# Performance work log

Hardware: AMD Instinct MI355X
Metric: run time of the kernel (lower is better)

## Reference

```python
import jax, jax.numpy as jnp
import numpy as np
import math

N_NODES = 50000
N_EDGES = 800000
IN_CH = 128
HID_CH = 16   # per-head channels of conv1
OUT_CH = 1    # per-head channels of conv2 (forced so Linear(heads,100) type-checks)
HEADS = 8


def _seg_softmax(scores, seg, n):
    # softmax over edges grouped by target node (variable-size neighborhoods)
    m = jax.ops.segment_max(scores, seg, num_segments=n)
    e = jnp.exp(scores - m[seg])
    s = jax.ops.segment_sum(e, seg, num_segments=n)
    return e / (s[seg] + 1e-16)


def _transformer_conv(x, edge_index, Wq, bq, Wk, bk, Wv, bv, Ws, bs, heads, ch):
    # PyG TransformerConv, concat=True, root_weight=True, beta=False
    n = x.shape[0]
    src, dst = edge_index[0], edge_index[1]
    q = (x @ Wq + bq).reshape(n, heads, ch)
    k = (x @ Wk + bk).reshape(n, heads, ch)
    v = (x @ Wv + bv).reshape(n, heads, ch)
    qi = q[dst]              # [E, H, C] gather at target
    kj = k[src]              # [E, H, C] gather at source
    vj = v[src]              # [E, H, C]
    alpha = jnp.einsum('ehc,ehc->eh', qi, kj) / math.sqrt(ch)  # [E, H]
    alpha = _seg_softmax(alpha, dst, n)
    agg = jax.ops.segment_sum(vj * alpha[:, :, None], dst, num_segments=n)
    out = agg.reshape(n, heads * ch)
    return out + x @ Ws + bs   # skip connection lin_skip(x)


def setup_inputs() -> dict:
    key = jax.random.key(0)
    ks = jax.random.split(key, 16)
    s = 0.05
    d1 = HEADS * HID_CH  # 128
    d2 = HEADS * OUT_CH  # 8
    inp = {
        'x': jax.random.normal(ks[0], (N_NODES, IN_CH), dtype=jnp.float32),
        'edge_index': jax.random.randint(ks[1], (2, N_EDGES), 0, N_NODES),
        # conv1 params
        'Wq1': jax.random.normal(ks[2], (IN_CH, d1), dtype=jnp.float32) * s,
        'bq1': jnp.zeros((d1,), jnp.float32),
        'Wk1': jax.random.normal(ks[3], (IN_CH, d1), dtype=jnp.float32) * s,
        'bk1': jnp.zeros((d1,), jnp.float32),
        'Wv1': jax.random.normal(ks[4], (IN_CH, d1), dtype=jnp.float32) * s,
        'bv1': jnp.zeros((d1,), jnp.float32),
        'Ws1': jax.random.normal(ks[5], (IN_CH, d1), dtype=jnp.float32) * s,
        'bs1': jnp.zeros((d1,), jnp.float32),
        # conv2 params (in = hidden*heads = 128)
        'Wq2': jax.random.normal(ks[6], (d1, d2), dtype=jnp.float32) * s,
        'bq2': jnp.zeros((d2,), jnp.float32),
        'Wk2': jax.random.normal(ks[7], (d1, d2), dtype=jnp.float32) * s,
        'bk2': jnp.zeros((d2,), jnp.float32),
        'Wv2': jax.random.normal(ks[8], (d1, d2), dtype=jnp.float32) * s,
        'bv2': jnp.zeros((d2,), jnp.float32),
        'Ws2': jax.random.normal(ks[9], (d1, d2), dtype=jnp.float32) * s,
        'bs2': jnp.zeros((d2,), jnp.float32),
        # final linear: heads -> 100
        'Wl': jax.random.normal(ks[10], (HEADS, 100), dtype=jnp.float32) * s,
        'bl': jnp.zeros((100,), jnp.float32),
    }
    return inp


def reference(x, edge_index, Wq1, bq1, Wk1, bk1, Wv1, bv1, Ws1, bs1,
              Wq2, bq2, Wk2, bk2, Wv2, bv2, Ws2, bs2, Wl, bl):
    h = _transformer_conv(x, edge_index, Wq1, bq1, Wk1, bk1, Wv1, bv1, Ws1, bs1, HEADS, HID_CH)
    h = _transformer_conv(h, edge_index, Wq2, bq2, Wk2, bk2, Wv2, bv2, Ws2, bs2, HEADS, OUT_CH)
    h = jax.nn.relu(h @ Wl + bl)   # dropout is identity in eval mode
    return jnp.mean(h, axis=0, keepdims=True)   # [1, 100]
```

## Files before the change

kernel.cpp:

```cpp
#include <hip/hip_runtime.h>
#include <hip/hip_bf16.h>
#include <cstdint>
#include <cstddef>


typedef _Float16 f16x8 __attribute__((ext_vector_type(8)));
typedef _Float16 f16x4 __attribute__((ext_vector_type(4)));
typedef _Float16 f16x2 __attribute__((ext_vector_type(2)));
typedef float    f32x4 __attribute__((ext_vector_type(4)));
typedef float    f32x2 __attribute__((ext_vector_type(2)));

__global__ __launch_bounds__(256) void pack_weights(
    const float* __restrict__ Wq1, const float* __restrict__ bq1,
    const float* __restrict__ Wk1, const float* __restrict__ bk1,
    const float* __restrict__ Wv1, const float* __restrict__ bv1,
    const float* __restrict__ Ws1, const float* __restrict__ bs1,
    const float* __restrict__ Wq2, const float* __restrict__ bq2,
    const float* __restrict__ Wk2, const float* __restrict__ bk2,
    const float* __restrict__ Wv2, const float* __restrict__ bv2,
    const float* __restrict__ Ws2, const float* __restrict__ bs2,
    _Float16* __restrict__ Wt1, float* __restrict__ b1,
    _Float16* __restrict__ Wt2, float* __restrict__ b2)
{
    int i = blockIdx.x * 256 + threadIdx.x;
    if (i < 65536) {
        int j = i >> 7, k = i & 127;
        const float* W; int col; float sc = 1.f;
        if (j < 128)      { W = Wq1; col = j; sc = 0.25f; }
        else if (j < 384) { int t = j - 128, c = t >> 2, r = t & 3;
                            if (r < 2) { W = Wk1; col = 2 * c + r; }
                            else       { W = Wv1; col = 2 * c + r - 2; } }
        else              { W = Ws1; col = j - 384; }
        Wt1[i] = (_Float16)(W[k * 128 + col] * sc);
    } else if (i < 66048) {
        int j = i - 65536;
        const float* B; int col; float sc = 1.f;
        if (j < 128)      { B = bq1; col = j; sc = 0.25f; }
        else if (j < 384) { int t = j - 128, c = t >> 2, r = t & 3;
                            if (r < 2) { B = bk1; col = 2 * c + r; }
                            else       { B = bv1; col = 2 * c + r - 2; } }
        else              { B = bs1; col = j - 384; }
        b1[j] = B[col] * sc;
    } else if (i < 66048 + 4096) {
        int t = i - 66048;
        int j = t >> 7, k = t & 127;
        const float* W; int col;
        if (j < 8)       { W = Wq2; col = j; }
        else if (j < 24) { int u = j - 8; col = u >> 1; W = (u & 1) ? Wv2 : Wk2; }
        else             { W = Ws2; col = j - 24; }
        Wt2[t] = (_Float16)W[k * 8 + col];
    } else if (i < 66048 + 4096 + 32) {
        int j = i - (66048 + 4096);
        const float* B; int col;
        if (j < 8)       { B = bq2; col = j; }
        else if (j < 24) { int u = j - 8; col = u >> 1; B = (u & 1) ? bv2 : bk2; }
        else             { B = bs2; col = j - 24; }
        b2[j] = B[col];
    }
}

__global__ __launch_bounds__(256) void gemm1(
    const float* __restrict__ x, const _Float16* __restrict__ Wt1,
    const float* __restrict__ b1, _Float16* __restrict__ qs,
    unsigned char* __restrict__ kvbuf, int n)
{
    __shared__ _Float16 As[64][136];
    __shared__ _Float16 BD[64][136];
    int tid = threadIdx.x;
    int rowbase = blockIdx.x * 64;
    #pragma unroll
    for (int it = 0; it < 8; ++it) {
        int c = it * 256 + tid, row = c >> 5, ch = c & 31;
        float4 v = make_float4(0.f, 0.f, 0.f, 0.f);
        if (rowbase + row < n) v = *(const float4*)&x[(size_t)(rowbase + row) * 128 + ch * 4];
        f16x4 hv = { (_Float16)v.x, (_Float16)v.y, (_Float16)v.z, (_Float16)v.w };
        *(f16x4*)&As[row][ch * 4] = hv;
    }
    int w = tid >> 6, l = tid & 63;
    int wm = w >> 1, wn = w & 1, fr = l & 15, fg = l >> 4;
    for (int cb = 0; cb < 8; ++cb) {
        __syncthreads();
        #pragma unroll
        for (int it = 0; it < 4; ++it) {
            int c = it * 256 + tid, row = c >> 4, ch = c & 15;
            *(f16x8*)&BD[row][ch * 8] =
                *(const f16x8*)&Wt1[(size_t)(cb * 64 + row) * 128 + ch * 8];
        }
        __syncthreads();
        f32x4 acc[2][2] = {};
        #pragma unroll
        for (int kk = 0; kk < 4; ++kk) {
            int ko = kk * 32 + fg * 8;
            f16x8 a0 = *(const f16x8*)&As[wm * 32 + fr][ko];
            f16x8 a1 = *(const f16x8*)&As[wm * 32 + 16 + fr][ko];
            f16x8 b0 = *(const f16x8*)&BD[wn * 32 + fr][ko];
            f16x8 b1v = *(const f16x8*)&BD[wn * 32 + 16 + fr][ko];
            acc[0][0] = __builtin_amdgcn_mfma_f32_16x16x32_f16(a0, b0, acc[0][0], 0, 0, 0);
            acc[0][1] = __builtin_amdgcn_mfma_f32_16x16x32_f16(a0, b1v, acc[0][1], 0, 0, 0);
            acc[1][0] = __builtin_amdgcn_mfma_f32_16x16x32_f16(a1, b0, acc[1][0], 0, 0, 0);
            acc[1][1] = __builtin_amdgcn_mfma_f32_16x16x32_f16(a1, b1v, acc[1][1], 0, 0, 0);
        }
        __syncthreads();
        #pragma unroll
        for (int nt = 0; nt < 2; ++nt) {
            int col = wn * 32 + nt * 16 + fr;
            float bv = b1[cb * 64 + col];
            #pragma unroll
            for (int mt = 0; mt < 2; ++mt)
                #pragma unroll
                for (int r = 0; r < 4; ++r)
                    BD[wm * 32 + mt * 16 + fg * 4 + r][col] = (_Float16)(acc[mt][nt][r] + bv);
        }
        __syncthreads();
        if (cb >= 2 && cb < 6) {
            int row = tid >> 2, ch = tid & 3;
            if (rowbase + row < n) {
                f16x8 d0 = *(const f16x8*)&BD[row][ch * 16];
                f16x8 d1 = *(const f16x8*)&BD[row][ch * 16 + 8];
                int w0 = 0, w1 = 0, w2 = 0, w3 = 0;
                w0 = __builtin_amdgcn_cvt_pk_fp8_f32((float)d0[0], (float)d0[1], w0, false);
                w0 = __builtin_amdgcn_cvt_pk_fp8_f32((float)d0[2], (float)d0[3], w0, true);
                w1 = __builtin_amdgcn_cvt_pk_fp8_f32((float)d0[4], (float)d0[5], w1, false);
                w1 = __builtin_amdgcn_cvt_pk_fp8_f32((float)d0[6], (float)d0[7], w1, true);
                w2 = __builtin_amdgcn_cvt_pk_fp8_f32((float)d1[0], (float)d1[1], w2, false);
                w2 = __builtin_amdgcn_cvt_pk_fp8_f32((float)d1[2], (float)d1[3], w2, true);
                w3 = __builtin_amdgcn_cvt_pk_fp8_f32((float)d1[4], (float)d1[5], w3, false);
                w3 = __builtin_amdgcn_cvt_pk_fp8_f32((float)d1[6], (float)d1[7], w3, true);
                uint4 o = make_uint4((unsigned)w0, (unsigned)w1, (unsigned)w2, (unsigned)w3);
                *(uint4*)&kvbuf[(size_t)(rowbase + row) * 256 + (cb - 2) * 64 + ch * 16] = o;
            }
        } else {
            int dcol = (cb < 2) ? cb * 64 : (cb - 6) * 64 + 128;
            #pragma unroll
            for (int it = 0; it < 2; ++it) {
                int c = it * 256 + tid, row = c >> 3, ch = c & 7;
                if (rowbase + row < n)
                    *(f16x8*)&qs[(size_t)(rowbase + row) * 256 + dcol + ch * 8] =
                        *(const f16x8*)&BD[row][ch * 8];
            }
        }
    }
}

__global__ __launch_bounds__(256) void count_edges(
    const int* __restrict__ ei, int* __restrict__ counts, int E)
{
    int e = blockIdx.x * 256 + threadIdx.x;
    if (e < E) atomicAdd(&counts[ei[E + e]], 1);
}

__global__ __launch_bounds__(256) void scan1(
    const int* __restrict__ counts, int* __restrict__ indptr,
    int* __restrict__ blocksums, int n)
{
    int t = threadIdx.x, b = blockIdx.x, i = b * 256 + t;
    int v = (i < n) ? counts[i] : 0;
    int x = v;
    #pragma unroll
    for (int off = 1; off < 64; off <<= 1) {
        int y = __shfl_up(x, off, 64);
        if ((t & 63) >= off) x += y;
    }
    __shared__ int wsum[4];
    if ((t & 63) == 63) wsum[t >> 6] = x;
    __syncthreads();
    int woff = 0;
    for (int w = 0; w < (t >> 6); ++w) woff += wsum[w];
    if (i < n) indptr[i] = woff + x - v;
    if (t == 255) blocksums[b] = woff + x;
}

__global__ __launch_bounds__(256) void scan2(
    const int* __restrict__ blocksums, int* __restrict__ blockoff,
    int* __restrict__ indptr, int nb, int n, int E)
{
    int t = threadIdx.x;
    int v = (t < nb) ? blocksums[t] : 0;
    int x = v;
    #pragma unroll
    for (int off = 1; off < 64; off <<= 1) {
        int y = __shfl_up(x, off, 64);
        if ((t & 63) >= off) x += y;
    }
    __shared__ int wsum[4];
    if ((t & 63) == 63) wsum[t >> 6] = x;
    __syncthreads();
    int woff = 0;
    for (int w = 0; w < (t >> 6); ++w) woff += wsum[w];
    if (t < nb) blockoff[t] = woff + x - v;
    if (t == 0) indptr[n] = E;
}

__global__ __launch_bounds__(256) void scan3(
    int* __restrict__ indptr, const int* __restrict__ blockoff, int n)
{
    int i = blockIdx.x * 256 + threadIdx.x;
    if (i < n) indptr[i] += blockoff[blockIdx.x];
}

__global__ __launch_bounds__(256) void scatter_edges(
    const int* __restrict__ ei, const int* __restrict__ indptr,
    int* __restrict__ fill, int* __restrict__ srcs, int E)
{
    int e = blockIdx.x * 256 + threadIdx.x;
    if (e < E) {
        int d = ei[E + e];
        int pos = indptr[d] + atomicAdd(&fill[d], 1);
        srcs[pos] = ei[e];
    }
}

__global__ __launch_bounds__(256) void attn1(
    const _Float16* __restrict__ qs, const unsigned char* __restrict__ kvbuf,
    const int* __restrict__ indptr, const int* __restrict__ srcs,
    _Float16* __restrict__ h1, int n)
{
    int wid = threadIdx.x >> 6, l = threadIdx.x & 63;
    int node = blockIdx.x * 4 + wid;
    if (node >= n) return;
    int lam = l & 15, quarter = l >> 4;
    const _Float16* nrow = qs + (size_t)node * 256;
    f16x8 q8 = ((const f16x8*)nrow)[lam];
    float qf0 = (float)q8[0], qf1 = (float)q8[1], qf2 = (float)q8[2], qf3 = (float)q8[3];
    float qf4 = (float)q8[4], qf5 = (float)q8[5], qf6 = (float)q8[6], qf7 = (float)q8[7];
    float den = 0.f;
    float a0 = 0.f, a1 = 0.f, a2 = 0.f, a3 = 0.f;
    float a4 = 0.f, a5 = 0.f, a6 = 0.f, a7 = 0.f;
    int lane_off = lam * 16;

    auto edge = [&](uint4 kv, bool ok) {
        f32x2 k0 = __builtin_amdgcn_cvt_pk_f32_fp8((int)kv.x, false);
        f32x2 k1 = __builtin_amdgcn_cvt_pk_f32_fp8((int)kv.y, false);
        f32x2 k2 = __builtin_amdgcn_cvt_pk_f32_fp8((int)kv.z, false);
        f32x2 k3 = __builtin_amdgcn_cvt_pk_f32_fp8((int)kv.w, false);
        float p = k0.x * qf0 + k0.y * qf1 + k1.x * qf2 + k1.y * qf3
                + k2.x * qf4 + k2.y * qf5 + k3.x * qf6 + k3.y * qf7;
        p += __shfl_xor(p, 1, 64);
        float w = __expf(ok ? p : -1e30f);
        den += w;
        f32x2 v0 = __builtin_amdgcn_cvt_pk_f32_fp8((int)kv.x, true);
        f32x2 v1 = __builtin_amdgcn_cvt_pk_f32_fp8((int)kv.y, true);
        f32x2 v2 = __builtin_amdgcn_cvt_pk_f32_fp8((int)kv.z, true);
        f32x2 v3 = __builtin_amdgcn_cvt_pk_f32_fp8((int)kv.w, true);
        a0 = fmaf(w, v0.x, a0); a1 = fmaf(w, v0.y, a1);
        a2 = fmaf(w, v1.x, a2); a3 = fmaf(w, v1.y, a3);
        a4 = fmaf(w, v2.x, a4); a5 = fmaf(w, v2.y, a5);
        a6 = fmaf(w, v3.x, a6); a7 = fmaf(w, v3.y, a7);
    };

    int i0 = indptr[node], deg = indptr[node + 1] - i0;
    for (int base = 0; base < deg; base += 64) {
        int cnt = min(64, deg - base);
        int sv8 = 0;
        if (base + l < deg) sv8 = srcs[i0 + base + l] << 8;
        int e = 0;
        for (; e + 8 <= cnt; e += 8) {
            int oA = __shfl(sv8, e + quarter, 64);
            int oB = __shfl(sv8, e + 4 + quarter, 64);
            uint4 kvA = *(const uint4*)(kvbuf + oA + lane_off);
            uint4 kvB = *(const uint4*)(kvbuf + oB + lane_off);
            edge(kvA, true); edge(kvB, true);
        }
        for (; e < cnt; e += 4) {
            int idx = e + quarter;
            int o = __shfl(sv8, idx, 64);
            uint4 kv = *(const uint4*)(kvbuf + o + lane_off);
            edge(kv, idx < cnt);
        }
    }
    den += __shfl_xor(den, 16, 64); den += __shfl_xor(den, 32, 64);
    a0 += __shfl_xor(a0, 16, 64); a0 += __shfl_xor(a0, 32, 64);
    a1 += __shfl_xor(a1, 16, 64); a1 += __shfl_xor(a1, 32, 64);
    a2 += __shfl_xor(a2, 16, 64); a2 += __shfl_xor(a2, 32, 64);
    a3 += __shfl_xor(a3, 16, 64); a3 += __shfl_xor(a3, 32, 64);
    a4 += __shfl_xor(a4, 16, 64); a4 += __shfl_xor(a4, 32, 64);
    a5 += __shfl_xor(a5, 16, 64); a5 += __shfl_xor(a5, 32, 64);
    a6 += __shfl_xor(a6, 16, 64); a6 += __shfl_xor(a6, 32, 64);
    a7 += __shfl_xor(a7, 16, 64); a7 += __shfl_xor(a7, 32, 64);
    if (quarter == 0) {
        float inv = 1.f / (den + 1e-16f);
        f16x8 s8 = ((const f16x8*)(nrow + 128))[lam];
        f16x8 o;
        o[0] = (_Float16)fmaf(a0, inv, (float)s8[0]);
        o[1] = (_Float16)fmaf(a1, inv, (float)s8[1]);
        o[2] = (_Float16)fmaf(a2, inv, (float)s8[2]);
        o[3] = (_Float16)fmaf(a3, inv, (float)s8[3]);
        o[4] = (_Float16)fmaf(a4, inv, (float)s8[4]);
        o[5] = (_Float16)fmaf(a5, inv, (float)s8[5]);
        o[6] = (_Float16)fmaf(a6, inv, (float)s8[6]);
        o[7] = (_Float16)fmaf(a7, inv, (float)s8[7]);
        ((f16x8*)(h1 + (size_t)node * 128))[lam] = o;
    }
}

__global__ __launch_bounds__(256) void gemm2(
    const _Float16* __restrict__ h1, const _Float16* __restrict__ Wt2,
    const float* __restrict__ b2, _Float16* __restrict__ qkvs2, int n)
{
    __shared__ _Float16 As[64][136];
    __shared__ _Float16 Bs[32][136];
    int tid = threadIdx.x;
    int rowbase = blockIdx.x * 64;
    #pragma unroll
    for (int it = 0; it < 4; ++it) {
        int c = it * 256 + tid, row = c >> 4, ch = c & 15;
        f16x8 v = {};
        if (rowbase + row < n) v = *(const f16x8*)&h1[(size_t)(rowbase + row) * 128 + ch * 8];
        *(f16x8*)&As[row][ch * 8] = v;
    }
    #pragma unroll
    for (int it = 0; it < 2; ++it) {
        int c = it * 256 + tid, row = c >> 4, ch = c & 15;
        *(f16x8*)&Bs[row][ch * 8] = *(const f16x8*)&Wt2[row * 128 + ch * 8];
    }
    __syncthreads();
    int w = tid >> 6, l = tid & 63, fr = l & 15, fg = l >> 4;
    f32x4 acc[2] = {};
    #pragma unroll
    for (int kk = 0; kk < 4; ++kk) {
        int ko = kk * 32 + fg * 8;
        f16x8 a = *(const f16x8*)&As[w * 16 + fr][ko];
        f16x8 b0 = *(const f16x8*)&Bs[fr][ko];
        f16x8 b1v = *(const f16x8*)&Bs[16 + fr][ko];
        acc[0] = __builtin_amdgcn_mfma_f32_16x16x32_f16(a, b0, acc[0], 0, 0, 0);
        acc[1] = __builtin_amdgcn_mfma_f32_16x16x32_f16(a, b1v, acc[1], 0, 0, 0);
    }
    #pragma unroll
    for (int nt = 0; nt < 2; ++nt) {
        int col = nt * 16 + fr;
        float bv = b2[col];
        #pragma unroll
        for (int r = 0; r < 4; ++r) {
            int row = rowbase + w * 16 + fg * 4 + r;
            if (row < n) qkvs2[(size_t)row * 32 + col] = (_Float16)(acc[nt][r] + bv);
        }
    }
}

__global__ __launch_bounds__(256) void attn2(
    const _Float16* __restrict__ q2, const int* __restrict__ indptr,
    const int* __restrict__ srcs, float* __restrict__ h2, int n)
{
    int wid = threadIdx.x >> 6, l = threadIdx.x & 63;
    int node = blockIdx.x * 4 + wid;
    if (node >= n) return;
    int i = l >> 3, h = l & 7;
    const _Float16* base = q2 + (size_t)node * 32;
    float qh = (float)base[h];
    int i0 = indptr[node], i1 = indptr[node + 1];
    float den = 0.f, acc = 0.f;
    for (int p = i0 + i; p < i1; p += 8) {
        int s = srcs[p];
        f16x2 kv = ((const f16x2*)(q2 + (size_t)s * 32 + 8))[h];
        float w = __expf(qh * (float)kv.x);
        den += w;
        acc = fmaf(w, (float)kv.y, acc);
    }
    den += __shfl_xor(den, 8, 64); den += __shfl_xor(den, 16, 64); den += __shfl_xor(den, 32, 64);
    acc += __shfl_xor(acc, 8, 64); acc += __shfl_xor(acc, 16, 64); acc += __shfl_xor(acc, 32, 64);
    if (i == 0)
        h2[(size_t)node * 8 + h] = acc / (den + 1e-16f) + (float)base[24 + h];
}

__global__ __launch_bounds__(128) void final_reduce(
    const float* __restrict__ h2, const float* __restrict__ Wl,
    const float* __restrict__ bl, float* __restrict__ out, int n, int chunk)
{
    int j = threadIdx.x;
    bool act = j < 100;
    float wl[8] = {};
    float bj = 0.f;
    if (act) {
        #pragma unroll
        for (int t = 0; t < 8; ++t) wl[t] = Wl[t * 100 + j];
        bj = bl[j];
    }
    int lo = blockIdx.x * chunk, hi = min(n, lo + chunk);
    float acc = 0.f;
    for (int node = lo; node < hi; ++node) {
        const float* hr = h2 + (size_t)node * 8;
        float y = bj;
        #pragma unroll
        for (int t = 0; t < 8; ++t) y += hr[t] * wl[t];
        acc += fmaxf(y, 0.f);
    }
    if (act) atomicAdd(&out[j], acc * (1.f / (float)n));
}

extern "C" void kernel_launch(void* const* d_in, const int* in_sizes, int n_in,
                              void* d_out, int out_size, void* d_ws, size_t ws_size,
                              hipStream_t stream)
{
    const float* x   = (const float*)d_in[0];
    const int*   ei  = (const int*)d_in[1];
    const float* Wq1 = (const float*)d_in[2],  *bq1 = (const float*)d_in[3];
    const float* Wk1 = (const float*)d_in[4],  *bk1 = (const float*)d_in[5];
    const float* Wv1 = (const float*)d_in[6],  *bv1 = (const float*)d_in[7];
    const float* Ws1 = (const float*)d_in[8],  *bs1 = (const float*)d_in[9];
    const float* Wq2 = (const float*)d_in[10], *bq2 = (const float*)d_in[11];
    const float* Wk2 = (const float*)d_in[12], *bk2 = (const float*)d_in[13];
    const float* Wv2 = (const float*)d_in[14], *bv2 = (const float*)d_in[15];
    const float* Ws2 = (const float*)d_in[16], *bs2 = (const float*)d_in[17];
    const float* Wl  = (const float*)d_in[18], *bl  = (const float*)d_in[19];
    float* out = (float*)d_out;

    int n = in_sizes[0] / 128;
    int E = in_sizes[1] / 2;

    char* p = (char*)d_ws;
    auto take = [&](size_t bytes) -> void* {
        void* r = (void*)p;
        p += (bytes + 255) & ~(size_t)255;
        return r;
    };
    _Float16*      qs     = (_Float16*)take((size_t)n * 256 * 2);
    unsigned char* kvbuf  = (unsigned char*)take((size_t)n * 256);
    _Float16*      h1     = (_Float16*)take((size_t)n * 128 * 2);
    _Float16*      qkvs2  = (_Float16*)take((size_t)n * 32 * 2);
    float*         h2     = (float*)take((size_t)n * 8 * 4);
    _Float16*      Wt1    = (_Float16*)take(65536 * 2);
    float*         b1     = (float*)take(512 * 4);
    _Float16*      Wt2    = (_Float16*)take(4096 * 2);
    float*         b2     = (float*)take(32 * 4);
    size_t  cz     = ((size_t)n * 4 + 255) & ~(size_t)255;
    int*    counts = (int*)take(cz);
    int*    fill   = (int*)take(cz);
    int*    indptr = (int*)take((size_t)(n + 1) * 4);
    int*    srcs   = (int*)take((size_t)E * 4);
    int     nb     = (n + 255) / 256;
    int*    blocksums = (int*)take((size_t)nb * 4);
    int*    blockoff  = (int*)take((size_t)nb * 4);

    hipMemsetAsync(counts, 0, cz * 2, stream);
    hipMemsetAsync(out, 0, (size_t)out_size * 4, stream);

    pack_weights<<<(70176 + 255) / 256, 256, 0, stream>>>(
        Wq1, bq1, Wk1, bk1, Wv1, bv1, Ws1, bs1,
        Wq2, bq2, Wk2, bk2, Wv2, bv2, Ws2, bs2,
        Wt1, b1, Wt2, b2);

    count_edges<<<(E + 255) / 256, 256, 0, stream>>>(ei, counts, E);
    scan1<<<nb, 256, 0, stream>>>(counts, indptr, blocksums, n);
    scan2<<<1, 256, 0, stream>>>(blocksums, blockoff, indptr, nb, n, E);
    scan3<<<nb, 256, 0, stream>>>(indptr, blockoff, n);
    scatter_edges<<<(E + 255) / 256, 256, 0, stream>>>(ei, indptr, fill, srcs, E);

    gemm1<<<(n + 63) / 64, 256, 0, stream>>>(x, Wt1, b1, qs, kvbuf, n);
    attn1<<<(n + 3) / 4, 256, 0, stream>>>(qs, kvbuf, indptr, srcs, h1, n);
    gemm2<<<(n + 63) / 64, 256, 0, stream>>>(h1, Wt2, b2, qkvs2, n);
    attn2<<<(n + 3) / 4, 256, 0, stream>>>(qkvs2, indptr, srcs, h2, n);

    int chunk = (n + 255) / 256;
    final_reduce<<<256, 128, 0, stream>>>(h2, Wl, bl, out, n, chunk);
}
```

Measured before the change: 319.1 us.

## Build CSR with rank-based single atomic pass, single-block scan and 16-bit sources

The CSR construction is rewritten. A rank_edges kernel records each edge's atomic slot within its destination, so the later placement needs no second round of atomics. A single 1024-thread block replaces the three-kernel scan, and source ids are stored as 16-bit values, which halves srcs traffic in both attention kernels. Zeroing of counts and the output is folded into pack_weights, removing two memsets and the fill buffer. In exchange, the 16-bit ids and ranks only hold while node count and degree stay below 65536, and the single-block scan is serial and strided per thread.

```diff
diff --git a/kernel.cpp b/kernel.cpp
--- a/kernel.cpp
+++ b/kernel.cpp
@@ -20,9 +20,12 @@
     const float* __restrict__ Wv2, const float* __restrict__ bv2,
     const float* __restrict__ Ws2, const float* __restrict__ bs2,
     _Float16* __restrict__ Wt1, float* __restrict__ b1,
-    _Float16* __restrict__ Wt2, float* __restrict__ b2)
+    _Float16* __restrict__ Wt2, float* __restrict__ b2,
+    int* __restrict__ counts, float* __restrict__ out, int n, int out_size)
 {
     int i = blockIdx.x * 256 + threadIdx.x;
+    if (i < n) counts[i] = 0;
+    if (i < out_size) out[i] = 0.f;
     if (i < 65536) {
         int j = i >> 7, k = i & 127;
         const float* W; int col; float sc = 1.f;
@@ -59,6 +62,69 @@
     }
 }
 
+__global__ __launch_bounds__(256) void rank_edges(
+    const int* __restrict__ ei, int* __restrict__ counts,
+    unsigned short* __restrict__ rank, int E)
+{
+    int e0 = (blockIdx.x * 256 + threadIdx.x) * 4;
+    if (e0 + 4 <= E) {
+        int4 d4 = *(const int4*)&ei[E + e0];
+        int r0 = atomicAdd(&counts[d4.x], 1);
+        int r1 = atomicAdd(&counts[d4.y], 1);
+        int r2 = atomicAdd(&counts[d4.z], 1);
+        int r3 = atomicAdd(&counts[d4.w], 1);
+        ushort4 rr = make_ushort4((unsigned short)r0, (unsigned short)r1,
+                                  (unsigned short)r2, (unsigned short)r3);
+        *(ushort4*)&rank[e0] = rr;
+    } else {
+        for (int e = e0; e < E; ++e)
+            rank[e] = (unsigned short)atomicAdd(&counts[ei[E + e]], 1);
+    }
+}
+
+__global__ __launch_bounds__(1024) void scan_all(
+    const int* __restrict__ counts, int* __restrict__ indptr, int n, int E)
+{
+    int t = threadIdx.x, lane = t & 63;
+    int per = (n + 1023) / 1024;
+    int lo = t * per, hi = min(n, lo + per);
+    int s = 0;
+    for (int i = lo; i < hi; ++i) s += counts[i];
+    int x = s;
+    #pragma unroll
+    for (int off = 1; off < 64; off <<= 1) {
+        int y = __shfl_up(x, off, 64);
+        if (lane >= off) x += y;
+    }
+    __shared__ int ws[16];
+    if (lane == 63) ws[t >> 6] = x;
+    __syncthreads();
+    int woff = 0;
+    for (int w = 0; w < (t >> 6); ++w) woff += ws[w];
+    int run = woff + x - s;
+    for (int i = lo; i < hi; ++i) { indptr[i] = run; run += counts[i]; }
+    if (t == 0) indptr[n] = E;
+}
+
+__global__ __launch_bounds__(256) void place_edges(
+    const int* __restrict__ ei, const int* __restrict__ indptr,
+    const unsigned short* __restrict__ rank, unsigned short* __restrict__ srcs, int E)
+{
+    int e0 = (blockIdx.x * 256 + threadIdx.x) * 4;
+    if (e0 + 4 <= E) {
+        int4 s4 = *(const int4*)&ei[e0];
+        int4 d4 = *(const int4*)&ei[E + e0];
+        ushort4 r4 = *(const ushort4*)&rank[e0];
+        srcs[indptr[d4.x] + r4.x] = (unsigned short)s4.x;
+        srcs[indptr[d4.y] + r4.y] = (unsigned short)s4.y;
+        srcs[indptr[d4.z] + r4.z] = (unsigned short)s4.z;
+        srcs[indptr[d4.w] + r4.w] = (unsigned short)s4.w;
+    } else {
+        for (int e = e0; e < E; ++e)
+            srcs[indptr[ei[E + e]] + rank[e]] = (unsigned short)ei[e];
+    }
+}
+
 __global__ __launch_bounds__(256) void gemm1(
     const float* __restrict__ x, const _Float16* __restrict__ Wt1,
     const float* __restrict__ b1, _Float16* __restrict__ qs,
@@ -142,77 +208,9 @@
     }
 }
 
-__global__ __launch_bounds__(256) void count_edges(
-    const int* __restrict__ ei, int* __restrict__ counts, int E)
-{
-    int e = blockIdx.x * 256 + threadIdx.x;
-    if (e < E) atomicAdd(&counts[ei[E + e]], 1);
-}
-
-__global__ __launch_bounds__(256) void scan1(
-    const int* __restrict__ counts, int* __restrict__ indptr,
-    int* __restrict__ blocksums, int n)
-{
-    int t = threadIdx.x, b = blockIdx.x, i = b * 256 + t;
-    int v = (i < n) ? counts[i] : 0;
-    int x = v;
-    #pragma unroll
-    for (int off = 1; off < 64; off <<= 1) {
-        int y = __shfl_up(x, off, 64);
-        if ((t & 63) >= off) x += y;
-    }
-    __shared__ int wsum[4];
-    if ((t & 63) == 63) wsum[t >> 6] = x;
-    __syncthreads();
-    int woff = 0;
-    for (int w = 0; w < (t >> 6); ++w) woff += wsum[w];
-    if (i < n) indptr[i] = woff + x - v;
-    if (t == 255) blocksums[b] = woff + x;
-}
-
-__global__ __launch_bounds__(256) void scan2(
-    const int* __restrict__ blocksums, int* __restrict__ blockoff,
-    int* __restrict__ indptr, int nb, int n, int E)
-{
-    int t = threadIdx.x;
-    int v = (t < nb) ? blocksums[t] : 0;
-    int x = v;
-    #pragma unroll
-    for (int off = 1; off < 64; off <<= 1) {
-        int y = __shfl_up(x, off, 64);
-        if ((t & 63) >= off) x += y;
-    }
-    __shared__ int wsum[4];
-    if ((t & 63) == 63) wsum[t >> 6] = x;
-    __syncthreads();
-    int woff = 0;
-    for (int w = 0; w < (t >> 6); ++w) woff += wsum[w];
-    if (t < nb) blockoff[t] = woff + x - v;
-    if (t == 0) indptr[n] = E;
-}
-
-__global__ __launch_bounds__(256) void scan3(
-    int* __restrict__ indptr, const int* __restrict__ blockoff, int n)
-{
-    int i = blockIdx.x * 256 + threadIdx.x;
-    if (i < n) indptr[i] += blockoff[blockIdx.x];
-}
-
-__global__ __launch_bounds__(256) void scatter_edges(
-    const int* __restrict__ ei, const int* __restrict__ indptr,
-    int* __restrict__ fill, int* __restrict__ srcs, int E)
-{
-    int e = blockIdx.x * 256 + threadIdx.x;
-    if (e < E) {
-        int d = ei[E + e];
-        int pos = indptr[d] + atomicAdd(&fill[d], 1);
-        srcs[pos] = ei[e];
-    }
-}
-
 __global__ __launch_bounds__(256) void attn1(
     const _Float16* __restrict__ qs, const unsigned char* __restrict__ kvbuf,
-    const int* __restrict__ indptr, const int* __restrict__ srcs,
+    const int* __restrict__ indptr, const unsigned short* __restrict__ srcs,
     _Float16* __restrict__ h1, int n)
 {
     int wid = threadIdx.x >> 6, l = threadIdx.x & 63;
@@ -252,7 +250,7 @@
     for (int base = 0; base < deg; base += 64) {
         int cnt = min(64, deg - base);
         int sv8 = 0;
-        if (base + l < deg) sv8 = srcs[i0 + base + l] << 8;
+        if (base + l < deg) sv8 = ((int)srcs[i0 + base + l]) << 8;
         int e = 0;
         for (; e + 8 <= cnt; e += 8) {
             int oA = __shfl(sv8, e + quarter, 64);
@@ -339,7 +337,7 @@
 
 __global__ __launch_bounds__(256) void attn2(
     const _Float16* __restrict__ q2, const int* __restrict__ indptr,
-    const int* __restrict__ srcs, float* __restrict__ h2, int n)
+    const unsigned short* __restrict__ srcs, float* __restrict__ h2, int n)
 {
     int wid = threadIdx.x >> 6, l = threadIdx.x & 63;
     int node = blockIdx.x * 4 + wid;
@@ -413,37 +411,29 @@
         p += (bytes + 255) & ~(size_t)255;
         return r;
     };
-    _Float16*      qs     = (_Float16*)take((size_t)n * 256 * 2);
-    unsigned char* kvbuf  = (unsigned char*)take((size_t)n * 256);
-    _Float16*      h1     = (_Float16*)take((size_t)n * 128 * 2);
-    _Float16*      qkvs2  = (_Float16*)take((size_t)n * 32 * 2);
-    float*         h2     = (float*)take((size_t)n * 8 * 4);
-    _Float16*      Wt1    = (_Float16*)take(65536 * 2);
-    float*         b1     = (float*)take(512 * 4);
-    _Float16*      Wt2    = (_Float16*)take(4096 * 2);
-    float*         b2     = (float*)take(32 * 4);
-    size_t  cz     = ((size_t)n * 4 + 255) & ~(size_t)255;
-    int*    counts = (int*)take(cz);
-    int*    fill   = (int*)take(cz);
-    int*    indptr = (int*)take((size_t)(n + 1) * 4);
-    int*    srcs   = (int*)take((size_t)E * 4);
-    int     nb     = (n + 255) / 256;
-    int*    blocksums = (int*)take((size_t)nb * 4);
-    int*    blockoff  = (int*)take((size_t)nb * 4);
-
-    hipMemsetAsync(counts, 0, cz * 2, stream);
-    hipMemsetAsync(out, 0, (size_t)out_size * 4, stream);
-
-    pack_weights<<<(70176 + 255) / 256, 256, 0, stream>>>(
+    _Float16*       qs     = (_Float16*)take((size_t)n * 256 * 2);
+    unsigned char*  kvbuf  = (unsigned char*)take((size_t)n * 256);
+    _Float16*       h1     = (_Float16*)take((size_t)n * 128 * 2);
+    _Float16*       qkvs2  = (_Float16*)take((size_t)n * 32 * 2);
+    float*          h2     = (float*)take((size_t)n * 8 * 4);
+    _Float16*       Wt1    = (_Float16*)take(65536 * 2);
+    float*          b1     = (float*)take(512 * 4);
+    _Float16*       Wt2    = (_Float16*)take(4096 * 2);
+    float*          b2     = (float*)take(32 * 4);
+    int*            counts = (int*)take((size_t)n * 4);
+    int*            indptr = (int*)take((size_t)(n + 1) * 4);
+    unsigned short* rank   = (unsigned short*)take((size_t)E * 2);
+    unsigned short* srcs   = (unsigned short*)take((size_t)E * 2);
+
+    pack_weights<<<(70400 + 255) / 256, 256, 0, stream>>>(
         Wq1, bq1, Wk1, bk1, Wv1, bv1, Ws1, bs1,
         Wq2, bq2, Wk2, bk2, Wv2, bv2, Ws2, bs2,
-        Wt1, b1, Wt2, b2);
-
-    count_edges<<<(E + 255) / 256, 256, 0, stream>>>(ei, counts, E);
-    scan1<<<nb, 256, 0, stream>>>(counts, indptr, blocksums, n);
-    scan2<<<1, 256, 0, stream>>>(blocksums, blockoff, indptr, nb, n, E);
-    scan3<<<nb, 256, 0, stream>>>(indptr, blockoff, n);
-    scatter_edges<<<(E + 255) / 256, 256, 0, stream>>>(ei, indptr, fill, srcs, E);
+        Wt1, b1, Wt2, b2, counts, out, n, out_size);
+
+    int eb = (E / 4 + 255) / 256;
+    rank_edges<<<eb, 256, 0, stream>>>(ei, counts, rank, E);
+    scan_all<<<1, 1024, 0, stream>>>(counts, indptr, n, E);
+    place_edges<<<eb, 256, 0, stream>>>(ei, indptr, rank, srcs, E);
 
     gemm1<<<(n + 63) / 64, 256, 0, stream>>>(x, Wt1, b1, qs, kvbuf, n);
     attn1<<<(n + 3) / 4, 256, 0, stream>>>(qs, kvbuf, indptr, srcs, h1, n);
```

Result: slower. 350.9 us (+9.9%).
